# Kernel tuning notes

Hardware: AMD Instinct MI355X
Metric: run time of the kernel (lower is better)

## Reference

```python
import jax, jax.numpy as jnp
import numpy as np
import math

DIM = 4096
N_HEADS = 32
N_KV_HEADS = 8
HEAD_DIM = DIM // N_HEADS
N_REP = N_HEADS // N_KV_HEADS
ROPE_BASE = 10000.0


def apply_rotary_emb(x):
    # x: [b, s, h, d] -> rotate pairs (LLaMA-style complex rotation)
    b, s, h, d = x.shape
    inv_freq = 1.0 / (ROPE_BASE ** (jnp.arange(0, d, 2, dtype=jnp.float32) / d))  # [d/2]
    pos = jnp.arange(s, dtype=jnp.float32)
    ang = pos[:, None] * inv_freq[None, :]          # [s, d/2]
    cos = jnp.cos(ang)[None, :, None, :]            # [1, s, 1, d/2]
    sin = jnp.sin(ang)[None, :, None, :]
    xr = x.reshape(b, s, h, d // 2, 2)
    x0, x1 = xr[..., 0], xr[..., 1]
    out = jnp.stack([x0 * cos - x1 * sin, x0 * sin + x1 * cos], axis=-1)
    return out.reshape(b, s, h, d)


def setup_inputs() -> dict:
    key = jax.random.key(0)
    ks = jax.random.split(key, 5)
    sc = 1.0 / math.sqrt(DIM)
    return {
        "x": jax.random.normal(ks[0], (2, 2048, DIM), dtype=jnp.float32),
        "Wq": jax.random.normal(ks[1], (DIM, N_HEADS * HEAD_DIM), dtype=jnp.float32) * sc,
        "Wk": jax.random.normal(ks[2], (DIM, N_KV_HEADS * HEAD_DIM), dtype=jnp.float32) * sc,
        "Wv": jax.random.normal(ks[3], (DIM, N_KV_HEADS * HEAD_DIM), dtype=jnp.float32) * sc,
        "Wo": jax.random.normal(ks[4], (N_HEADS * HEAD_DIM, DIM), dtype=jnp.float32) * sc,
    }


def reference(x, Wq, Wk, Wv, Wo):
    b, s, _ = x.shape
    xq = (x @ Wq).reshape(b, s, N_HEADS, HEAD_DIM)
    xk = (x @ Wk).reshape(b, s, N_KV_HEADS, HEAD_DIM)
    xv = (x @ Wv).reshape(b, s, N_KV_HEADS, HEAD_DIM)
    xq = apply_rotary_emb(xq)
    xk = apply_rotary_emb(xk)
    # GQA: repeat kv heads
    xk = jnp.repeat(xk, N_REP, axis=2)  # [b, s, H, d]
    xv = jnp.repeat(xv, N_REP, axis=2)
    scores = jnp.einsum('bqhd,bkhd->bhqk', xq, xk) / math.sqrt(HEAD_DIM)
    causal = jnp.tril(jnp.ones((s, s), dtype=bool))
    scores = jnp.where(causal[None, None], scores, -jnp.inf)
    probs = jax.nn.softmax(scores.astype(jnp.float32), axis=-1).astype(xq.dtype)
    out = jnp.einsum('bhqk,bkhd->bqhd', probs, xv).reshape(b, s, N_HEADS * HEAD_DIM)
    return out @ Wo  # dropout is identity in eval
```

## Files before the change

### kernel.cpp

```cpp
#include <hip/hip_runtime.h>
#include <hip/hip_bf16.h>

typedef __attribute__((ext_vector_type(8))) short short8;
typedef __attribute__((ext_vector_type(4))) float f32x4;

typedef const void __attribute__((address_space(1)))* gptr_t;
typedef void __attribute__((address_space(3)))* sptr_t;

static __device__ __forceinline__ void gload_lds16(const void* g, void* l) {
  __builtin_amdgcn_global_load_lds((gptr_t)g, (sptr_t)l, 16, 0, 0);
}

static __device__ __forceinline__ unsigned short f2bf(float f) {
  unsigned int u = __float_as_uint(f);
  unsigned int r = (u + 0x7fffu + ((u >> 16) & 1u)) >> 16;
  return (unsigned short)r;
}
static __device__ __forceinline__ float bf2f(unsigned short b) {
  return __uint_as_float(((unsigned int)b) << 16);
}
static __device__ __forceinline__ unsigned int cvt_pk_bf16(float lo, float hi) {
  unsigned int r;
  asm("v_cvt_pk_bf16_f32 %0, %1, %2" : "=v"(r) : "v"(lo), "v"(hi));
  return r;
}

__global__ void cvt_f32_to_bf16(const float* __restrict__ in,
                                unsigned short* __restrict__ out, int n) {
  int idx = blockIdx.x * blockDim.x + threadIdx.x;
  int stride = gridDim.x * blockDim.x;
  for (int i = idx * 4; i < n; i += stride * 4) {
    const float4 v = *reinterpret_cast<const float4*>(in + i);
    unsigned long long packed =
        (unsigned long long)f2bf(v.x) | ((unsigned long long)f2bf(v.y) << 16) |
        ((unsigned long long)f2bf(v.z) << 32) | ((unsigned long long)f2bf(v.w) << 48);
    *reinterpret_cast<unsigned long long*>(out + i) = packed;
  }
}

__global__ void cvt_transpose_bf16(const float* __restrict__ in,
                                   unsigned short* __restrict__ out, int K, int N) {
  __shared__ unsigned short tile[32][33];
  int kt = blockIdx.y * 32, nt = blockIdx.x * 32;
  int tx = threadIdx.x & 31;
  int ty = threadIdx.x >> 5;
  #pragma unroll
  for (int i = 0; i < 32; i += 8)
    tile[ty + i][tx] = f2bf(in[(size_t)(kt + ty + i) * N + nt + tx]);
  __syncthreads();
  #pragma unroll
  for (int i = 0; i < 32; i += 8)
    out[(size_t)(nt + ty + i) * K + kt + tx] = tile[tx][ty + i];
}

__global__ void transpose_v(const unsigned short* __restrict__ Vp,
                            unsigned short* __restrict__ VT, int vstride) {
  __shared__ unsigned short tile[32][33];
  int st = blockIdx.x * 32;
  int dt = blockIdx.y * 32;
  int bh = blockIdx.z;
  int b = bh >> 3, h = bh & 7;
  int tx = threadIdx.x & 31, ty = threadIdx.x >> 5;
  #pragma unroll
  for (int i = 0; i < 32; i += 8)
    tile[ty + i][tx] = Vp[(size_t)(b * 2048 + st + ty + i) * vstride + h * 128 + dt + tx];
  __syncthreads();
  #pragma unroll
  for (int i = 0; i < 32; i += 8)
    VT[(size_t)((b * 8 + h) * 128 + dt + ty + i) * 2048 + st + tx] = tile[tx][ty + i];
}

__global__ void rope_kernel(unsigned short* __restrict__ buf, int rows, int nheads,
                            int rowstride, float oscale) {
  int total = rows * nheads * 64;
  int idx = blockIdx.x * blockDim.x + threadIdx.x;
  if (idx >= total) return;
  int j = idx & 63;
  int hh = (idx >> 6) % nheads;
  int r = idx / (64 * nheads);
  int pos = r & 2047;
  float inv = expf(-(float)j * 0.14391157f);
  float ang = (float)pos * inv;
  float s, c;
  sincosf(ang, &s, &c);
  unsigned int* p =
      reinterpret_cast<unsigned int*>(buf + (size_t)r * rowstride + hh * 128 + 2 * j);
  unsigned int pv = *p;
  float x0 = bf2f((unsigned short)(pv & 0xffffu));
  float x1 = bf2f((unsigned short)(pv >> 16));
  float o0 = (x0 * c - x1 * s) * oscale;
  float o1 = (x0 * s + x1 * c) * oscale;
  *p = (unsigned int)f2bf(o0) | ((unsigned int)f2bf(o1) << 16);
}

static __device__ __forceinline__ void store_out(unsigned short* C, size_t idx, float v) {
  C[idx] = f2bf(v);
}
static __device__ __forceinline__ void store_out(float* C, size_t idx, float v) {
  C[idx] = v;
}

template <typename OutT>
__global__ __launch_bounds__(512) void gemm_bt256(const unsigned short* __restrict__ A,
                                                  const unsigned short* __restrict__ BT,
                                                  OutT* __restrict__ C, int M, int N,
                                                  int K) {
  __shared__ __align__(16) unsigned short S[4][16384];
  const int tid = threadIdx.x;
  const int w = tid >> 6, lane = tid & 63;
  const int fr = lane & 15, fg = lane >> 4;
  const int wr = w >> 2, wc = w & 3;

  const int nbx = N >> 8;
  const int bid = blockIdx.x;
  const int cpx = gridDim.x >> 3;
  const int lid = (bid & 7) * cpx + (bid >> 3);
  const int brow = lid / nbx, bcol = lid % nbx;

  const int srl = lane >> 2;
  const int scc = (lane & 3) ^ (((lane >> 5) & 1) << 1);
  const unsigned short* gA = A + (size_t)(brow * 256) * K;
  const unsigned short* gB = BT + (size_t)(bcol * 256) * K;

  f32x4 acc[8][4] = {};
  const int rdoff = fr * 32 + ((fg ^ (((fr >> 3) & 1) << 1)) * 8);

  const int NT = K >> 5;

  for (int s = 0; s < 3; s++) {
    const int kb = s * 32;
    #pragma unroll
    for (int u = 0; u < 2; u++) {
      int sb = 2 * w + u;
      gload_lds16(gA + (size_t)(sb * 16 + srl) * K + kb + scc * 8, &S[s][sb * 512]);
    }
    #pragma unroll
    for (int u = 0; u < 2; u++) {
      int sb = 2 * w + u;
      gload_lds16(gB + (size_t)(sb * 16 + srl) * K + kb + scc * 8, &S[s][8192 + sb * 512]);
    }
  }
  asm volatile("s_waitcnt vmcnt(8)" ::: "memory");
  __builtin_amdgcn_s_barrier();

  for (int s = 0; s < NT; s++) {
    const unsigned short* Sa = &S[s & 3][0];
    const unsigned short* Sb = &S[s & 3][8192];
    const int bufn = (s + 3) & 3;
    int kn = s + 3;
    if (kn >= NT) kn -= NT;
    const int kbn = kn * 32;

    short8 b[4], a0[4];
    #pragma unroll
    for (int j = 0; j < 4; j++)
      b[j] = *reinterpret_cast<const short8*>(&Sb[(wc * 4 + j) * 512 + rdoff]);
    #pragma unroll
    for (int i = 0; i < 4; i++)
      a0[i] = *reinterpret_cast<const short8*>(&Sa[(wr * 8 + i) * 512 + rdoff]);
    #pragma unroll
    for (int u = 0; u < 2; u++) {
      int sb = 2 * w + u;
      gload_lds16(gA + (size_t)(sb * 16 + srl) * K + kbn + scc * 8, &S[bufn][sb * 512]);
    }
    __builtin_amdgcn_s_barrier();
    asm volatile("s_waitcnt lgkmcnt(0)" ::: "memory");
    __builtin_amdgcn_sched_barrier(0);
    __builtin_amdgcn_s_setprio(1);
    #pragma unroll
    for (int i = 0; i < 4; i++)
      #pragma unroll
      for (int j = 0; j < 4; j++)
        acc[i][j] = __builtin_amdgcn_mfma_f32_16x16x32_bf16(a0[i], b[j], acc[i][j], 0, 0, 0);
    __builtin_amdgcn_s_setprio(0);
    __builtin_amdgcn_s_barrier();

    short8 a1[4];
    #pragma unroll
    for (int i = 0; i < 4; i++)
      a1[i] = *reinterpret_cast<const short8*>(&Sa[(wr * 8 + 4 + i) * 512 + rdoff]);
    #pragma unroll
    for (int u = 0; u < 2; u++) {
      int sb = 2 * w + u;
      gload_lds16(gB + (size_t)(sb * 16 + srl) * K + kbn + scc * 8,
                  &S[bufn][8192 + sb * 512]);
    }
    __builtin_amdgcn_s_barrier();
    asm volatile("s_waitcnt lgkmcnt(0)" ::: "memory");
    __builtin_amdgcn_sched_barrier(0);
    __builtin_amdgcn_s_setprio(1);
    #pragma unroll
    for (int i = 0; i < 4; i++)
      #pragma unroll
      for (int j = 0; j < 4; j++)
        acc[4 + i][j] =
            __builtin_amdgcn_mfma_f32_16x16x32_bf16(a1[i], b[j], acc[4 + i][j], 0, 0, 0);
    __builtin_amdgcn_s_setprio(0);
    asm volatile("s_waitcnt vmcnt(8)" ::: "memory");
    __builtin_amdgcn_s_barrier();
  }

  #pragma unroll
  for (int i = 0; i < 8; i++)
    #pragma unroll
    for (int j = 0; j < 4; j++)
      #pragma unroll
      for (int r = 0; r < 4; r++) {
        int row = brow * 256 + wr * 128 + i * 16 + fg * 4 + r;
        int col = bcol * 256 + wc * 64 + j * 16 + fr;
        store_out(C, (size_t)row * N + col, acc[i][j][r]);
      }
}

__global__ __launch_bounds__(256, 2) void flash_attn(const unsigned short* __restrict__ Q,
                                                     const unsigned short* __restrict__ KV,
                                                     const unsigned short* __restrict__ VT,
                                                     unsigned short* __restrict__ O) {
  __shared__ __align__(16) unsigned short K_lds[2][64][128];
  __shared__ __align__(16) unsigned short V_lds[2][128][64];
  __shared__ __align__(16) unsigned short P_lds[4][16][68];

  const int wave = threadIdx.x >> 6, lane = threadIdx.x & 63;
  const int fr = lane & 15, fg = lane >> 4;

  const int bid = blockIdx.x;
  const int lid = (bid & 7) * 64 + (bid >> 3);
  const int pr = lid & 7;
  const int h = (lid >> 3) & 31;
  const int b = lid >> 8;
  const int kvh = h >> 2;

  const unsigned short* Qb = Q + (size_t)(b * 2048) * 4096 + h * 128;
  const unsigned short* Kb = KV + (size_t)(b * 2048) * 2048 + kvh * 128;
  const unsigned short* Vb = VT + (size_t)((b * 8 + kvh) * 128) * 2048;

  const int l4 = lane >> 4, c16 = lane & 15;
  const int l3 = lane >> 3, c8 = lane & 7;

  auto stage = [&](int kb, int bf) {
    #pragma unroll
    for (int c = 0; c < 4; c++) {
      int rl = wave * 16 + c * 4 + l4;
      int ch = c16 ^ (rl & 7);
      gload_lds16(Kb + (size_t)(kb + rl) * 2048 + ch * 8, &K_lds[bf][wave * 16 + c * 4][0]);
    }
    #pragma unroll
    for (int c = 0; c < 4; c++) {
      int rl = wave * 32 + c * 8 + l3;
      int ch = c8 ^ (rl & 7);
      gload_lds16(Vb + (size_t)rl * 2048 + kb + ch * 8, &V_lds[bf][wave * 32 + c * 8][0]);
    }
  };

  for (int seg = 0; seg < 2; seg++) {
    const int blk = seg ? pr : 15 - pr;
    const int qw = blk * 128 + wave * 32;

    short8 qf[2][4];
    #pragma unroll
    for (int m = 0; m < 2; m++)
      #pragma unroll
      for (int dk = 0; dk < 4; dk++)
        qf[m][dk] = *reinterpret_cast<const short8*>(
            &Qb[(size_t)(qw + m * 16 + fr) * 4096 + dk * 32 + fg * 8]);

    float mrow[2] = {-INFINITY, -INFINITY};
    float lrow[2] = {0.f, 0.f};
    f32x4 oacc[2][8] = {};

    const int nt = 2 * blk + 2;
    stage(0, 0);

    for (int t = 0; t < nt; t++) {
      const int kb = t * 64;
      if (t + 1 < nt) {
        stage((t + 1) * 64, (t + 1) & 1);
        asm volatile("s_waitcnt vmcnt(8)" ::: "memory");
      } else {
        asm volatile("s_waitcnt vmcnt(0)" ::: "memory");
      }
      __builtin_amdgcn_s_barrier();

      if (kb <= qw + 31) {
        const unsigned short* Kl = &K_lds[t & 1][0][0];
        const unsigned short* Vl = &V_lds[t & 1][0][0];

        f32x4 s[2][4] = {};
        #pragma unroll
        for (int kc = 0; kc < 4; kc++) {
          short8 kf[4];
          #pragma unroll
          for (int dk = 0; dk < 4; dk++)
            kf[dk] = *reinterpret_cast<const short8*>(
                &Kl[(kc * 16 + fr) * 128 + (((dk * 4 + fg) ^ (fr & 7)) << 3)]);
          #pragma unroll
          for (int dk = 0; dk < 4; dk++) {
            s[0][kc] =
                __builtin_amdgcn_mfma_f32_16x16x32_bf16(kf[dk], qf[0][dk], s[0][kc], 0, 0, 0);
            s[1][kc] =
                __builtin_amdgcn_mfma_f32_16x16x32_bf16(kf[dk], qf[1][dk], s[1][kc], 0, 0, 0);
          }
        }
        if (kb + 63 > qw) {
          #pragma unroll
          for (int m = 0; m < 2; m++) {
            const int qi = qw + m * 16 + fr;
            #pragma unroll
            for (int kc = 0; kc < 4; kc++)
              #pragma unroll
              for (int r = 0; r < 4; r++)
                if (kb + kc * 16 + fg * 4 + r > qi) s[m][kc][r] = -INFINITY;
          }
        }

        short8 pf[2][2];
        #pragma unroll
        for (int m = 0; m < 2; m++) {
          float mx = -INFINITY;
          #pragma unroll
          for (int kc = 0; kc < 4; kc++)
            #pragma unroll
            for (int r = 0; r < 4; r++) mx = fmaxf(mx, s[m][kc][r]);
          mx = fmaxf(mx, __shfl_xor(mx, 16));
          mx = fmaxf(mx, __shfl_xor(mx, 32));
          const bool need = !__all(mx - mrow[m] <= 8.0f);
          float mnew = need ? fmaxf(mrow[m], mx) : mrow[m];
          if (need) {
            float alpha = exp2f(mrow[m] - mnew);
            lrow[m] *= alpha;
            float alw[4];
            #pragma unroll
            for (int r = 0; r < 4; r++) alw[r] = __shfl(alpha, fg * 4 + r);
            #pragma unroll
            for (int dt = 0; dt < 8; dt++)
              #pragma unroll
              for (int r = 0; r < 4; r++) oacc[m][dt][r] *= alw[r];
          }
          float p_[16];
          float rs = 0.f;
          #pragma unroll
          for (int kc = 0; kc < 4; kc++)
            #pragma unroll
            for (int r = 0; r < 4; r++) {
              float pv = exp2f(s[m][kc][r] - mnew);
              p_[kc * 4 + r] = pv;
              rs += pv;
            }
          rs += __shfl_xor(rs, 16);
          rs += __shfl_xor(rs, 32);
          lrow[m] += rs;
          mrow[m] = mnew;
          #pragma unroll
          for (int kc = 0; kc < 4; kc++) {
            unsigned int lo = cvt_pk_bf16(p_[kc * 4 + 0], p_[kc * 4 + 1]);
            unsigned int hi = cvt_pk_bf16(p_[kc * 4 + 2], p_[kc * 4 + 3]);
            unsigned int* dst =
                reinterpret_cast<unsigned int*>(&P_lds[wave][fr][kc * 16 + fg * 4]);
            dst[0] = lo;
            dst[1] = hi;
          }
          pf[m][0] = *reinterpret_cast<const short8*>(&P_lds[wave][fr][fg * 8]);
          pf[m][1] = *reinterpret_cast<const short8*>(&P_lds[wave][fr][32 + fg * 8]);
        }

        #pragma unroll
        for (int c = 0; c < 2; c++)
          #pragma unroll
          for (int dt = 0; dt < 8; dt++) {
            short8 vf = *reinterpret_cast<const short8*>(
                &Vl[(dt * 16 + fr) * 64 + (((c * 4 + fg) ^ (fr & 7)) << 3)]);
            oacc[0][dt] =
                __builtin_amdgcn_mfma_f32_16x16x32_bf16(pf[0][c], vf, oacc[0][dt], 0, 0, 0);
            oacc[1][dt] =
                __builtin_amdgcn_mfma_f32_16x16x32_bf16(pf[1][c], vf, oacc[1][dt], 0, 0, 0);
          }
      }
      __builtin_amdgcn_s_barrier();
    }

    #pragma unroll
    for (int m = 0; m < 2; m++) {
      float linv[4];
      #pragma unroll
      for (int r = 0; r < 4; r++) linv[r] = 1.0f / __shfl(lrow[m], fg * 4 + r);
      #pragma unroll
      for (int dt = 0; dt < 8; dt++)
        #pragma unroll
        for (int r = 0; r < 4; r++) {
          int row = qw + m * 16 + fg * 4 + r;
          float v = oacc[m][dt][r] * linv[r];
          O[(size_t)(b * 2048 + row) * 4096 + h * 128 + dt * 16 + fr] = f2bf(v);
        }
    }
  }
}

extern "C" void kernel_launch(void* const* d_in, const int* in_sizes, int n_in,
                              void* d_out, int out_size, void* d_ws, size_t ws_size,
                              hipStream_t stream) {
  const float* x = (const float*)d_in[0];
  const float* Wq = (const float*)d_in[1];
  const float* Wk = (const float*)d_in[2];
  const float* Wv = (const float*)d_in[3];
  const float* Wo = (const float*)d_in[4];
  float* out = (float*)d_out;

  char* ws = (char*)d_ws;
  unsigned short* xb   = (unsigned short*)(ws + 0);
  unsigned short* WqT  = (unsigned short*)(ws + 33554432);
  unsigned short* WkvT = (unsigned short*)(ws + 67108864);
  unsigned short* WoT  = (unsigned short*)(ws + 83886080);
  unsigned short* Qb   = (unsigned short*)(ws + 117440512);
  unsigned short* KVb  = (unsigned short*)(ws + 150994944);
  unsigned short* VT   = (unsigned short*)(ws + 167772160);
  unsigned short* Ob   = (unsigned short*)(ws + 176160768);

  cvt_f32_to_bf16<<<2048, 256, 0, stream>>>(x, xb, 4096 * 4096);
  cvt_transpose_bf16<<<dim3(128, 128), 256, 0, stream>>>(Wq, WqT, 4096, 4096);
  cvt_transpose_bf16<<<dim3(32, 128), 256, 0, stream>>>(Wk, WkvT, 4096, 1024);
  cvt_transpose_bf16<<<dim3(32, 128), 256, 0, stream>>>(Wv, WkvT + (size_t)1024 * 4096,
                                                        4096, 1024);
  cvt_transpose_bf16<<<dim3(128, 128), 256, 0, stream>>>(Wo, WoT, 4096, 4096);

  gemm_bt256<unsigned short><<<256, 512, 0, stream>>>(xb, WqT, Qb, 4096, 4096, 4096);
  gemm_bt256<unsigned short><<<128, 512, 0, stream>>>(xb, WkvT, KVb, 4096, 2048, 4096);

  rope_kernel<<<(4096 * 32 * 64 + 255) / 256, 256, 0, stream>>>(Qb, 4096, 32, 4096,
                                                                0.12751780f);
  rope_kernel<<<(4096 * 8 * 64 + 255) / 256, 256, 0, stream>>>(KVb, 4096, 8, 2048, 1.0f);

  transpose_v<<<dim3(64, 4, 16), 256, 0, stream>>>(KVb + 1024, VT, 2048);

  flash_attn<<<512, 256, 0, stream>>>(Qb, KVb, VT, Ob);

  gemm_bt256<float><<<256, 512, 0, stream>>>(Ob, WoT, out, 4096, 4096, 4096);
}
```

Baseline: 550.7 us.

## Template GEMM on A-tile height and restructure inner loop barriers

The GEMM kernel is templated on the A-tile height, so the KV projection can use 128x256 tiles and launch 256 blocks instead of 128, filling more compute units. The main loop is also restructured: all A and B fragments are read from LDS up front and both global-to-LDS prefetches are issued together. The mid-iteration barriers are replaced by partial lgkmcnt waits, so the second MFMA half can overlap outstanding LDS reads. In exchange, the smaller tile gives less reuse per block, and dropping barriers risks ordering issues with the LDS ring buffer.

New measurement: 516.3 us (median of 2 runs). 6.2% less time.

```diff
diff --git a/kernel.cpp b/kernel.cpp
--- a/kernel.cpp
+++ b/kernel.cpp
@@ -100,12 +100,13 @@
   C[idx] = v;
 }
 
-template <typename OutT>
+template <int AM, typename OutT>
 __global__ __launch_bounds__(512) void gemm_bt256(const unsigned short* __restrict__ A,
                                                   const unsigned short* __restrict__ BT,
                                                   OutT* __restrict__ C, int M, int N,
                                                   int K) {
-  __shared__ __align__(16) unsigned short S[4][16384];
+  constexpr int H = AM / 4;
+  __shared__ __align__(16) unsigned short S[4][(AM + 16) * 512];
   const int tid = threadIdx.x;
   const int w = tid >> 6, lane = tid & 63;
   const int fr = lane & 15, fg = lane >> 4;
@@ -119,10 +120,10 @@
 
   const int srl = lane >> 2;
   const int scc = (lane & 3) ^ (((lane >> 5) & 1) << 1);
-  const unsigned short* gA = A + (size_t)(brow * 256) * K;
+  const unsigned short* gA = A + (size_t)(brow * (AM * 16)) * K;
   const unsigned short* gB = BT + (size_t)(bcol * 256) * K;
 
-  f32x4 acc[8][4] = {};
+  f32x4 acc[2 * H][4] = {};
   const int rdoff = fr * 32 + ((fg ^ (((fr >> 3) & 1) << 1)) * 8);
 
   const int NT = K >> 5;
@@ -130,83 +131,89 @@
   for (int s = 0; s < 3; s++) {
     const int kb = s * 32;
     #pragma unroll
+    for (int u = 0; u < AM / 8; u++) {
+      int sb = (AM / 8) * w + u;
+      gload_lds16(gA + (size_t)(sb * 16 + srl) * K + kb + scc * 8, &S[s][sb * 512]);
+    }
+    #pragma unroll
     for (int u = 0; u < 2; u++) {
       int sb = 2 * w + u;
-      gload_lds16(gA + (size_t)(sb * 16 + srl) * K + kb + scc * 8, &S[s][sb * 512]);
-    }
-    #pragma unroll
-    for (int u = 0; u < 2; u++) {
-      int sb = 2 * w + u;
-      gload_lds16(gB + (size_t)(sb * 16 + srl) * K + kb + scc * 8, &S[s][8192 + sb * 512]);
+      gload_lds16(gB + (size_t)(sb * 16 + srl) * K + kb + scc * 8,
+                  &S[s][AM * 512 + sb * 512]);
     }
   }
-  asm volatile("s_waitcnt vmcnt(8)" ::: "memory");
+  if constexpr (AM == 16)
+    asm volatile("s_waitcnt vmcnt(8)" ::: "memory");
+  else
+    asm volatile("s_waitcnt vmcnt(6)" ::: "memory");
   __builtin_amdgcn_s_barrier();
 
   for (int s = 0; s < NT; s++) {
     const unsigned short* Sa = &S[s & 3][0];
-    const unsigned short* Sb = &S[s & 3][8192];
+    const unsigned short* Sb = &S[s & 3][AM * 512];
     const int bufn = (s + 3) & 3;
     int kn = s + 3;
     if (kn >= NT) kn -= NT;
     const int kbn = kn * 32;
 
-    short8 b[4], a0[4];
+    short8 b[4], a0[H], a1[H];
     #pragma unroll
     for (int j = 0; j < 4; j++)
       b[j] = *reinterpret_cast<const short8*>(&Sb[(wc * 4 + j) * 512 + rdoff]);
     #pragma unroll
-    for (int i = 0; i < 4; i++)
-      a0[i] = *reinterpret_cast<const short8*>(&Sa[(wr * 8 + i) * 512 + rdoff]);
+    for (int i = 0; i < H; i++)
+      a0[i] = *reinterpret_cast<const short8*>(&Sa[(wr * 2 * H + i) * 512 + rdoff]);
+    #pragma unroll
+    for (int i = 0; i < H; i++)
+      a1[i] = *reinterpret_cast<const short8*>(&Sa[(wr * 2 * H + H + i) * 512 + rdoff]);
+    #pragma unroll
+    for (int u = 0; u < AM / 8; u++) {
+      int sb = (AM / 8) * w + u;
+      gload_lds16(gA + (size_t)(sb * 16 + srl) * K + kbn + scc * 8, &S[bufn][sb * 512]);
+    }
     #pragma unroll
     for (int u = 0; u < 2; u++) {
       int sb = 2 * w + u;
-      gload_lds16(gA + (size_t)(sb * 16 + srl) * K + kbn + scc * 8, &S[bufn][sb * 512]);
-    }
-    __builtin_amdgcn_s_barrier();
+      gload_lds16(gB + (size_t)(sb * 16 + srl) * K + kbn + scc * 8,
+                  &S[bufn][AM * 512 + sb * 512]);
+    }
+    if constexpr (AM == 16)
+      asm volatile("s_waitcnt lgkmcnt(4)" ::: "memory");
+    else
+      asm volatile("s_waitcnt lgkmcnt(2)" ::: "memory");
+    __builtin_amdgcn_sched_barrier(0);
+    __builtin_amdgcn_s_setprio(1);
+    #pragma unroll
+    for (int i = 0; i < H; i++)
+      #pragma unroll
+      for (int j = 0; j < 4; j++)
+        acc[i][j] = __builtin_amdgcn_mfma_f32_16x16x32_bf16(a0[i], b[j], acc[i][j], 0, 0, 0);
+    __builtin_amdgcn_s_setprio(0);
+    __builtin_amdgcn_sched_barrier(0);
     asm volatile("s_waitcnt lgkmcnt(0)" ::: "memory");
     __builtin_amdgcn_sched_barrier(0);
     __builtin_amdgcn_s_setprio(1);
     #pragma unroll
-    for (int i = 0; i < 4; i++)
+    for (int i = 0; i < H; i++)
       #pragma unroll
       for (int j = 0; j < 4; j++)
-        acc[i][j] = __builtin_amdgcn_mfma_f32_16x16x32_bf16(a0[i], b[j], acc[i][j], 0, 0, 0);
+        acc[H + i][j] =
+            __builtin_amdgcn_mfma_f32_16x16x32_bf16(a1[i], b[j], acc[H + i][j], 0, 0, 0);
     __builtin_amdgcn_s_setprio(0);
-    __builtin_amdgcn_s_barrier();
-
-    short8 a1[4];
-    #pragma unroll
-    for (int i = 0; i < 4; i++)
-      a1[i] = *reinterpret_cast<const short8*>(&Sa[(wr * 8 + 4 + i) * 512 + rdoff]);
-    #pragma unroll
-    for (int u = 0; u < 2; u++) {
-      int sb = 2 * w + u;
-      gload_lds16(gB + (size_t)(sb * 16 + srl) * K + kbn + scc * 8,
-                  &S[bufn][8192 + sb * 512]);
-    }
-    __builtin_amdgcn_s_barrier();
-    asm volatile("s_waitcnt lgkmcnt(0)" ::: "memory");
-    __builtin_amdgcn_sched_barrier(0);
-    __builtin_amdgcn_s_setprio(1);
-    #pragma unroll
-    for (int i = 0; i < 4; i++)
-      #pragma unroll
-      for (int j = 0; j < 4; j++)
-        acc[4 + i][j] =
-            __builtin_amdgcn_mfma_f32_16x16x32_bf16(a1[i], b[j], acc[4 + i][j], 0, 0, 0);
-    __builtin_amdgcn_s_setprio(0);
-    asm volatile("s_waitcnt vmcnt(8)" ::: "memory");
+    if constexpr (AM == 16)
+      asm volatile("s_waitcnt vmcnt(8)" ::: "memory");
+    else
+      asm volatile("s_waitcnt vmcnt(6)" ::: "memory");
     __builtin_amdgcn_s_barrier();
   }
 
   #pragma unroll
-  for (int i = 0; i < 8; i++)
+  for (int i = 0; i < 2 * H; i++)
     #pragma unroll
     for (int j = 0; j < 4; j++)
       #pragma unroll
       for (int r = 0; r < 4; r++) {
-        int row = brow * 256 + wr * 128 + i * 16 + fg * 4 + r;
+        int row = brow * (AM * 16) + wr * (AM * 8) + i * 16 + fg * 4 + r;
         int col = bcol * 256 + wc * 64 + j * 16 + fr;
         store_out(C, (size_t)row * N + col, acc[i][j][r]);
       }
@@ -422,8 +429,8 @@
                                                         4096, 1024);
   cvt_transpose_bf16<<<dim3(128, 128), 256, 0, stream>>>(Wo, WoT, 4096, 4096);
 
-  gemm_bt256<unsigned short><<<256, 512, 0, stream>>>(xb, WqT, Qb, 4096, 4096, 4096);
-  gemm_bt256<unsigned short><<<128, 512, 0, stream>>>(xb, WkvT, KVb, 4096, 2048, 4096);
+  gemm_bt256<16, unsigned short><<<256, 512, 0, stream>>>(xb, WqT, Qb, 4096, 4096, 4096);
+  gemm_bt256<8, unsigned short><<<256, 512, 0, stream>>>(xb, WkvT, KVb, 4096, 2048, 4096);
 
   rope_kernel<<<(4096 * 32 * 64 + 255) / 256, 256, 0, stream>>>(Qb, 4096, 32, 4096,
                                                                 0.12751780f);
@@ -433,5 +440,5 @@
 
   flash_attn<<<512, 256, 0, stream>>>(Qb, KVb, VT, Ob);
 
-  gemm_bt256<float><<<256, 512, 0, stream>>>(Ob, WoT, out, 4096, 4096, 4096);
-}
+  gemm_bt256<16, float><<<256, 512, 0, stream>>>(Ob, WoT, out, 4096, 4096, 4096);
+}
```
